# Optimization experiments

Measured on AMD Instinct MI355X. Metric: run time of the kernel, lower is better.

## Reference

```python
import jax, jax.numpy as jnp
import numpy as np
from jax import lax

L, B, S, D, V, NL = 64, 32, 64, 512, 32000, 2


def setup_inputs() -> dict:
    key = jax.random.key(0)
    ks = jax.random.split(key, 9)
    sd = 1.0 / np.sqrt(D)
    return {
        "rnn_input": jax.random.randint(ks[0], (L, B), 0, V),
        "last_hidden": jax.random.normal(ks[1], (NL, B, D), jnp.float32),
        "encoder_outputs": jax.random.normal(ks[2], (S, B, D), jnp.float32),
        "embed_table": jax.random.normal(ks[3], (V, D), jnp.float32) * sd,
        "sru_W": jax.random.normal(ks[4], (NL, D, 3 * D), jnp.float32) * sd,
        "sru_b": jax.random.normal(ks[5], (NL, 2 * D), jnp.float32) * 0.01,
        "attn_W": jax.random.normal(ks[6], (2 * D, D), jnp.float32) * sd,
        "out_W": jax.random.normal(ks[7], (D, V), jnp.float32) * sd,
        "out_b": jax.random.normal(ks[8], (V,), jnp.float32) * 0.01,
    }


def _sru_layer(x, c0, W, b):
    # x: [L,B,D] layer input, c0: [B,D], W: [D,3D], b: [2D]
    U = jnp.einsum('lbd,de->lbe', x, W)          # [L,B,3D]
    z, fp, rp = jnp.split(U, 3, axis=-1)          # candidate, forget, reset pre-acts
    bf, br = jnp.split(b, 2)
    f = jax.nn.sigmoid(fp + bf)
    r = jax.nn.sigmoid(rp + br)

    def step(c, inp):
        f_t, z_t = inp
        c = f_t * c + (1.0 - f_t) * z_t
        return c, c

    c_last, c_seq = lax.scan(step, c0, (f, z))    # c_seq: [L,B,D]
    h = r * jnp.tanh(c_seq) + (1.0 - r) * x       # highway (n_in == n_out)
    return h, c_last


def reference(rnn_input, last_hidden, encoder_outputs, embed_table, sru_W, sru_b, attn_W, out_W, out_b):
    x = embed_table[rnn_input]                    # [L,B,D]
    finals = []
    for l in range(NL):                           # small fixed layer loop
        x, c_last = _sru_layer(x, last_hidden[l], sru_W[l], sru_b[l])
        finals.append(c_last)
    hidden = jnp.stack(finals, axis=0)            # [NL,B,D]

    q = jnp.transpose(x, (1, 0, 2))               # [B,L,D]
    mem = jnp.transpose(encoder_outputs, (1, 0, 2))  # [B,S,D]
    scores = jnp.einsum('bld,bsd->bls', q, mem)   # dot attention
    align = jax.nn.softmax(scores, axis=-1)
    ctx = jnp.einsum('bls,bsd->bld', align, mem)
    attn_h = jnp.tanh(jnp.concatenate([ctx, q], axis=-1) @ attn_W)  # [B,L,D]
    output = attn_h @ out_W + out_b               # [B,L,V]
    return output, hidden
```

## Files before the change

### kernel.cpp

```cpp
#include <hip/hip_runtime.h>
#include <hip/hip_bf16.h>

#define L_ 64
#define B_ 32
#define S_ 64
#define D_ 512
#define V_ 32000
#define NL_ 2

typedef __attribute__((ext_vector_type(8))) short bf16x8;
typedef __attribute__((ext_vector_type(4))) float f32x4;

static __device__ __forceinline__ short f2bf(float f) {
  union { float f; unsigned u; } x; x.f = f;
  unsigned r = (x.u + 0x7FFFu + ((x.u >> 16) & 1u)) >> 16;
  return (short)r;
}

#define GLOAD_LDS16(g, l)                                                     \
  __builtin_amdgcn_global_load_lds(                                           \
      (const __attribute__((address_space(1))) void*)(g),                     \
      (__attribute__((address_space(3))) void*)(l), 16, 0, 0)

__global__ void embed_kernel(const int* __restrict__ tok, const float* __restrict__ tab,
                             float* __restrict__ xf, short* __restrict__ xb) {
  int i = blockIdx.x * 256 + threadIdx.x;
  int d = i & (D_ - 1);
  int lb = i >> 9;
  float v = tab[(size_t)tok[lb] * D_ + d];
  xf[i] = v;
  xb[i] = f2bf(v);
}

__global__ void transpose_f32_bf16(const float* __restrict__ in, short* __restrict__ out,
                                   int K, int N) {
  __shared__ float tile[32][33];
  int x = blockIdx.x * 32 + threadIdx.x;
  int y0 = blockIdx.y * 32;
  for (int j = threadIdx.y; j < 32; j += 8) {
    int y = y0 + j;
    tile[j][threadIdx.x] = (x < N && y < K) ? in[(size_t)y * N + x] : 0.f;
  }
  __syncthreads();
  int xo = y0 + threadIdx.x;
  int yo0 = blockIdx.x * 32;
  for (int j = threadIdx.y; j < 32; j += 8) {
    int yo = yo0 + j;
    if (yo < N && xo < K) out[(size_t)yo * K + xo] = f2bf(tile[threadIdx.x][j]);
  }
}

#define BM 128
#define BN 128
#define BK 64

template <int MODE>
__global__ __launch_bounds__(256) void gemm_kernel(
    const short* __restrict__ A, const short* __restrict__ BT,
    void* __restrict__ Cptr, const float* __restrict__ bias,
    int M, int N, int K, int nbm) {
  const int nwg = gridDim.x;
  const int qc = nwg >> 3;
  const int bid = blockIdx.x;
  const int wg = (bid & 7) * qc + (bid >> 3);
  const int bm = wg % nbm;
  const int bn = wg / nbm;

  __shared__ __align__(16) short la[2][BM * BK];
  __shared__ __align__(16) short lb[2][BN * BK];
  const int tid = threadIdx.x;
  const int wave = tid >> 6, lane = tid & 63;
  const int wm = (wave >> 1) * 64, wn = (wave & 1) * 64;

  f32x4 acc[4][4] = {};

  const int lrow = lane >> 3;
  const int lslot = lane & 7;
  const short* Abase = A + (size_t)(bm * BM) * K;
  const short* Bbase = BT + (size_t)(bn * BN) * K;

  auto stage = [&](int buf, int k0) {
#pragma unroll
    for (int c = 0; c < 4; ++c) {
      int chunk = wave * 4 + c;
      int row = chunk * 8 + lrow;
      int slot = lslot ^ (row & 7);
      GLOAD_LDS16(Abase + (size_t)row * K + k0 + slot * 8, &la[buf][chunk * 512]);
      GLOAD_LDS16(Bbase + (size_t)row * K + k0 + slot * 8, &lb[buf][chunk * 512]);
    }
  };

  stage(0, 0);
  __syncthreads();

  const int nt = K / BK;
  int cur = 0;
  for (int t = 0; t < nt; ++t) {
    if (t + 1 < nt) stage(cur ^ 1, (t + 1) * BK);
#pragma unroll
    for (int kk = 0; kk < 2; ++kk) {
      bf16x8 af[4], bfr[4];
#pragma unroll
      for (int mi = 0; mi < 4; ++mi) {
        int row = wm + mi * 16 + (lane & 15);
        int slot = (kk * 4 + (lane >> 4)) ^ (row & 7);
        af[mi] = *(const bf16x8*)&la[cur][row * 64 + slot * 8];
      }
#pragma unroll
      for (int ni = 0; ni < 4; ++ni) {
        int row = wn + ni * 16 + (lane & 15);
        int slot = (kk * 4 + (lane >> 4)) ^ (row & 7);
        bfr[ni] = *(const bf16x8*)&lb[cur][row * 64 + slot * 8];
      }
#pragma unroll
      for (int mi = 0; mi < 4; ++mi)
#pragma unroll
        for (int ni = 0; ni < 4; ++ni)
          acc[mi][ni] = __builtin_amdgcn_mfma_f32_16x16x32_bf16(
              af[mi], bfr[ni], acc[mi][ni], 0, 0, 0);
    }
    __syncthreads();
    cur ^= 1;
  }

  const int cl = lane & 15;
  const int rl = (lane >> 4) * 4;
#pragma unroll
  for (int mi = 0; mi < 4; ++mi) {
#pragma unroll
    for (int ni = 0; ni < 4; ++ni) {
      int c = bn * BN + wn + ni * 16 + cl;
      int r0 = bm * BM + wm + mi * 16 + rl;
#pragma unroll
      for (int j = 0; j < 4; ++j) {
        int r = r0 + j;
        float v = acc[mi][ni][j];
        if (MODE == 0) {
          ((float*)Cptr)[(size_t)r * N + c] = v;
        } else if (MODE == 1) {
          ((short*)Cptr)[(size_t)r * N + c] = f2bf(tanhf(v));
        } else {
          int b = r & 31, l = r >> 5;
          ((float*)Cptr)[(size_t)(b * L_ + l) * N + c] = v + bias[c];
        }
      }
    }
  }
}

__global__ void sru_scan_kernel(const float* __restrict__ U, const float* __restrict__ bvec,
                                const float* __restrict__ xin, const float* __restrict__ c0,
                                float* __restrict__ hf, short* __restrict__ hb,
                                float* __restrict__ clast) {
  int idx = blockIdx.x * 64 + threadIdx.x;
  int b = idx >> 9, d = idx & 511;
  float c = c0[idx];
  const float bfb = bvec[d], brb = bvec[512 + d];
  const float* Ub = U + (size_t)b * 1536 + d;
  const float* Xb = xin + (size_t)b * 512 + d;

  for (int l0 = 0; l0 < L_; l0 += 8) {
    float z[8], fp[8], rp[8], xv[8];
#pragma unroll
    for (int j = 0; j < 8; ++j) {
      size_t u = (size_t)(l0 + j) * B_ * 1536;
      z[j] = Ub[u];
      fp[j] = Ub[u + 512];
      rp[j] = Ub[u + 1024];
      xv[j] = Xb[(size_t)(l0 + j) * B_ * 512];
    }
#pragma unroll
    for (int j = 0; j < 8; ++j) {
      float f = 1.f / (1.f + expf(-(fp[j] + bfb)));
      float r = 1.f / (1.f + expf(-(rp[j] + brb)));
      c = f * c + (1.f - f) * z[j];
      float h = r * tanhf(c) + (1.f - r) * xv[j];
      size_t o = ((size_t)(l0 + j) * B_ + b) * 512 + d;
      hf[o] = h;
      hb[o] = f2bf(h);
    }
  }
  clast[idx] = c;
}

__global__ __launch_bounds__(256) void attn_fused_kernel(
    const float* __restrict__ x, const float* __restrict__ enc,
    const short* __restrict__ xq, short* __restrict__ cat) {
  __shared__ float q[512];
  __shared__ float al[64];
  int r = blockIdx.x;
  int b = r & (B_ - 1);
  int tid = threadIdx.x;
  int wave = tid >> 6, lane = tid & 63;
  for (int d = tid; d < 512; d += 256) {
    q[d] = x[(size_t)r * 512 + d];
    cat[(size_t)r * 1024 + 512 + d] = xq[(size_t)r * 512 + d];
  }
  __syncthreads();
#pragma unroll
  for (int si = 0; si < 16; ++si) {
    int s = wave * 16 + si;
    const float* m = enc + ((size_t)s * B_ + b) * 512;
    float a = 0.f;
#pragma unroll
    for (int k = 0; k < 8; ++k) a += q[lane + k * 64] * m[lane + k * 64];
    for (int o = 32; o > 0; o >>= 1) a += __shfl_xor(a, o);
    if (lane == 0) al[s] = a;
  }
  __syncthreads();
  if (tid < 64) {
    float v = al[tid];
    float mx = v;
    for (int o = 32; o > 0; o >>= 1) mx = fmaxf(mx, __shfl_xor(mx, o));
    float e = expf(v - mx);
    float sm = e;
    for (int o = 32; o > 0; o >>= 1) sm += __shfl_xor(sm, o);
    al[tid] = e / sm;
  }
  __syncthreads();
  for (int d = tid; d < 512; d += 256) {
    float acc = 0.f;
#pragma unroll 16
    for (int s = 0; s < S_; ++s) acc += al[s] * enc[((size_t)s * B_ + b) * 512 + d];
    cat[(size_t)r * 1024 + d] = f2bf(acc);
  }
}

extern "C" void kernel_launch(void* const* d_in, const int* in_sizes, int n_in,
                              void* d_out, int out_size, void* d_ws, size_t ws_size,
                              hipStream_t stream) {
  const int* rnn = (const int*)d_in[0];
  const float* h0 = (const float*)d_in[1];
  const float* enc = (const float*)d_in[2];
  const float* tab = (const float*)d_in[3];
  const float* sruW = (const float*)d_in[4];
  const float* srub = (const float*)d_in[5];
  const float* attnW = (const float*)d_in[6];
  const float* outW = (const float*)d_in[7];
  const float* outb = (const float*)d_in[8];
  float* out = (float*)d_out;

  char* ws = (char*)d_ws;
  size_t off = 0;
  auto alloc = [&](size_t bytes) {
    char* p = ws + off;
    off += (bytes + 255) & ~(size_t)255;
    return p;
  };
  float* xf = (float*)alloc(4ull * 2048 * 512);
  float* xf2 = (float*)alloc(4ull * 2048 * 512);
  short* xb = (short*)alloc(2ull * 2048 * 512);
  float* U = (float*)alloc(4ull * 2048 * 1536);
  short* WTs = (short*)alloc(2ull * 2 * 1536 * 512);
  short* WTa = (short*)alloc(2ull * 512 * 1024);
  short* WTo = (short*)alloc(2ull * 32000 * 512);
  short* cat = (short*)alloc(2ull * 2048 * 1024);
  short* ah = (short*)alloc(2ull * 2048 * 512);

  dim3 tb(32, 8);
  for (int l = 0; l < NL_; ++l)
    transpose_f32_bf16<<<dim3(48, 16), tb, 0, stream>>>(
        sruW + (size_t)l * 512 * 1536, WTs + (size_t)l * 1536 * 512, 512, 1536);
  transpose_f32_bf16<<<dim3(16, 32), tb, 0, stream>>>(attnW, WTa, 1024, 512);
  transpose_f32_bf16<<<dim3(1000, 16), tb, 0, stream>>>(outW, WTo, 512, 32000);

  embed_kernel<<<4096, 256, 0, stream>>>(rnn, tab, xf, xb);

  float* hidden_out = out + (size_t)B_ * L_ * V_;

  gemm_kernel<0><<<192, 256, 0, stream>>>(xb, WTs, U, nullptr, 2048, 1536, 512, 16);
  sru_scan_kernel<<<256, 64, 0, stream>>>(U, srub, xf, h0, xf2, xb, hidden_out);
  gemm_kernel<0><<<192, 256, 0, stream>>>(xb, WTs + 1536 * 512, U, nullptr, 2048, 1536, 512, 16);
  sru_scan_kernel<<<256, 64, 0, stream>>>(U, srub + 1024, xf2, h0 + B_ * D_, xf, xb,
                                          hidden_out + B_ * D_);

  attn_fused_kernel<<<2048, 256, 0, stream>>>(xf, enc, xb, cat);

  gemm_kernel<1><<<64, 256, 0, stream>>>(cat, WTa, ah, nullptr, 2048, 512, 1024, 16);
  gemm_kernel<2><<<4000, 256, 0, stream>>>(ah, WTo, out, outb, 2048, 32000, 512, 16);
}
```

Baseline: 274.6 us.

## Add 256x256-tile GEMM with 4-stage LDS pipeline for vocab projection

Adds a new GEMM kernel with 256x256 output tiles, 8 waves per block, a 4-slot global-to-LDS async ring with XOR-swizzled layout, and an XCD-aware block remap. It is used for the 2048x32000x512 output projection in place of the 128-tile kernel. The larger tile raises operand reuse per LDS load and cuts global traffic. The cost is higher register pressure (128 accumulator floats per lane) and fewer blocks, 1000, to fill the device.

```diff
diff --git a/kernel.cpp b/kernel.cpp
--- a/kernel.cpp
+++ b/kernel.cpp
@@ -137,11 +137,123 @@
         float v = acc[mi][ni][j];
         if (MODE == 0) {
           ((float*)Cptr)[(size_t)r * N + c] = v;
-        } else if (MODE == 1) {
+        } else {
           ((short*)Cptr)[(size_t)r * N + c] = f2bf(tanhf(v));
+        }
+      }
+    }
+  }
+}
+
+#define BM2 256
+#define BN2 256
+#define BK2 32
+
+template <int MODE>
+__global__ __launch_bounds__(512, 2) void gemm256_kernel(
+    const short* __restrict__ A, const short* __restrict__ BT,
+    void* __restrict__ Cptr, const float* __restrict__ bias,
+    int M, int N, int K, int nbm) {
+  const int nwg = gridDim.x;
+  const int qc = nwg >> 3;
+  const int bid = blockIdx.x;
+  const int wg = (bid & 7) * qc + (bid >> 3);
+  const int bm = wg % nbm;
+  const int bn = wg / nbm;
+
+  __shared__ __align__(16) short la[4][BM2 * BK2];
+  __shared__ __align__(16) short lb[4][BN2 * BK2];
+
+  const int tid = threadIdx.x;
+  const int wave = tid >> 6, lane = tid & 63;
+  const int wmb = (wave >> 2) * 128;
+  const int wnb = (wave & 3) * 64;
+
+  f32x4 acc[8][4] = {};
+
+  const short* Abase = A + (size_t)(bm * BM2) * K;
+  const short* Bbase = BT + (size_t)(bn * BN2) * K;
+  const int nt = K / BK2;
+
+  auto stage = [&](int slot, int t) {
+    const int k0 = t * BK2;
+#pragma unroll
+    for (int i = 0; i < 2; ++i) {
+      int p = i * 64 + (tid >> 3);
+      int u = (tid & 7) ^ (p & 7);
+      int row = 2 * p + (u >> 2);
+      int kq = u & 3;
+      GLOAD_LDS16(Abase + (size_t)row * K + k0 + kq * 8, &la[slot][i * 4096 + tid * 8]);
+    }
+#pragma unroll
+    for (int i = 0; i < 2; ++i) {
+      int p = i * 64 + (tid >> 3);
+      int u = (tid & 7) ^ (p & 7);
+      int row = 2 * p + (u >> 2);
+      int kq = u & 3;
+      GLOAD_LDS16(Bbase + (size_t)row * K + k0 + kq * 8, &lb[slot][i * 4096 + tid * 8]);
+    }
+  };
+
+  stage(0, 0);
+  stage(1, 1);
+  stage(2, 2);
+  asm volatile("s_waitcnt vmcnt(8)\n\ts_barrier" ::: "memory");
+
+  const int kq = lane >> 4;
+  const int fr = lane & 15;
+  int aoff[8], boff[4];
+#pragma unroll
+  for (int mi = 0; mi < 8; ++mi) {
+    int r = wmb + mi * 16 + fr;
+    aoff[mi] = (r >> 1) * 64 + (((((r & 1) << 2) | kq) ^ ((r >> 1) & 7)) << 3);
+  }
+#pragma unroll
+  for (int ni = 0; ni < 4; ++ni) {
+    int r = wnb + ni * 16 + fr;
+    boff[ni] = (r >> 1) * 64 + (((((r & 1) << 2) | kq) ^ ((r >> 1) & 7)) << 3);
+  }
+
+  for (int t = 0; t < nt; ++t) {
+    const int cur = t & 3;
+    if (t + 3 < nt) stage((t + 3) & 3, t + 3);
+    bf16x8 bfrag[4];
+#pragma unroll
+    for (int ni = 0; ni < 4; ++ni) bfrag[ni] = *(const bf16x8*)&lb[cur][boff[ni]];
+#pragma unroll
+    for (int mi = 0; mi < 8; ++mi) {
+      bf16x8 af = *(const bf16x8*)&la[cur][aoff[mi]];
+#pragma unroll
+      for (int ni = 0; ni < 4; ++ni)
+        acc[mi][ni] = __builtin_amdgcn_mfma_f32_16x16x32_bf16(af, bfrag[ni], acc[mi][ni], 0, 0, 0);
+    }
+    if (t < nt - 1) {
+      if (t + 3 < nt) {
+        asm volatile("s_waitcnt vmcnt(8)\n\ts_barrier" ::: "memory");
+      } else if (t + 2 < nt) {
+        asm volatile("s_waitcnt vmcnt(4)\n\ts_barrier" ::: "memory");
+      } else {
+        asm volatile("s_waitcnt vmcnt(0)\n\ts_barrier" ::: "memory");
+      }
+    }
+  }
+
+#pragma unroll
+  for (int mi = 0; mi < 8; ++mi) {
+#pragma unroll
+    for (int ni = 0; ni < 4; ++ni) {
+      int c = bn * BN2 + wnb + ni * 16 + fr;
+      int r0 = bm * BM2 + wmb + mi * 16 + (lane >> 4) * 4;
+      float bs = (MODE == 2) ? bias[c] : 0.f;
+#pragma unroll
+      for (int j = 0; j < 4; ++j) {
+        int r = r0 + j;
+        float v = acc[mi][ni][j];
+        if (MODE == 2) {
+          int b = r & 31, l = r >> 5;
+          ((float*)Cptr)[(size_t)(b * L_ + l) * N + c] = v + bs;
         } else {
-          int b = r & 31, l = r >> 5;
-          ((float*)Cptr)[(size_t)(b * L_ + l) * N + c] = v + bias[c];
+          ((float*)Cptr)[(size_t)r * N + c] = v;
         }
       }
     }
@@ -277,5 +389,5 @@
   attn_fused_kernel<<<2048, 256, 0, stream>>>(xf, enc, xb, cat);
 
   gemm_kernel<1><<<64, 256, 0, stream>>>(cat, WTa, ah, nullptr, 2048, 512, 1024, 16);
-  gemm_kernel<2><<<4000, 256, 0, stream>>>(ah, WTo, out, outb, 2048, 32000, 512, 16);
-}
+  gemm256_kernel<2><<<1000, 512, 0, stream>>>(ah, WTo, out, outb, 2048, 32000, 512, 8);
+}
```

After: 285.6 us. 1.04x slower.
